# Performance work log

Hardware: AMD Instinct MI355X
Metric: run time of the kernel (lower is better)

Reference implementation:

```python
import jax, jax.numpy as jnp
import numpy as np

HID, H, D = 128, 4, 32
NB, NP, NC = 60000, 2000, 4000
EM, EP, EI = 150000, 300000, 150000


def segment_softmax(logits, seg, n):
    # logits: [E, H], seg: [E] destination ids
    m = jax.ops.segment_max(logits, seg, num_segments=n)
    m = jnp.where(jnp.isfinite(m), m, 0.0)  # guard empty segments
    e = jnp.exp(logits - m[seg])
    s = jax.ops.segment_sum(e, seg, num_segments=n)
    return e / (s[seg] + 1e-16)


def layer_norm(x, g, b):
    mu = x.mean(-1, keepdims=True)
    v = ((x - mu) ** 2).mean(-1, keepdims=True)
    return (x - mu) / jnp.sqrt(v + 1e-5) * g + b


def setup_inputs():
    key = jax.random.key(0)
    ks = jax.random.split(key, 40)
    i = iter(range(40))
    nrm = lambda shape, s=1.0: jax.random.normal(ks[next(i)], shape, jnp.float32) * s
    w = lambda shape: nrm(shape, 0.05)
    inp = {
        'x_ball': nrm((NB, HID)),
        'x_player': nrm((NP, HID)),
        'x_context': nrm((NC, HID)),
        'em': jnp.stack([jax.random.randint(ks[next(i)], (EM,), 0, NP),
                         jax.random.randint(ks[next(i)], (EM,), 0, NB)]),
        'ep': jnp.stack([jax.random.randint(ks[next(i)], (EP,), 0, NB),
                         jax.random.randint(ks[next(i)], (EP,), 0, NB)]),
        'ei': jnp.stack([jax.random.randint(ks[next(i)], (EI,), 0, NB),
                         jax.random.randint(ks[next(i)], (EI,), 0, NC)]),
        'ea_p': nrm((EP, 1)),
        # GATv2Conv (player -matchup-> ball)
        'g_Wl': w((HID, HID)), 'g_Wr': w((HID, HID)), 'g_att': w((H, D)), 'g_b': jnp.zeros((HID,), jnp.float32),
        # TransformerConv (ball -recent_precedes-> ball), edge_dim=1
        't_Wq': w((HID, HID)), 't_bq': jnp.zeros((HID,), jnp.float32),
        't_Wk': w((HID, HID)), 't_bk': jnp.zeros((HID,), jnp.float32),
        't_Wv': w((HID, HID)), 't_bv': jnp.zeros((HID,), jnp.float32),
        't_We': w((1, HID)),
        't_Wskip': w((HID, HID)), 't_bskip': jnp.zeros((HID,), jnp.float32),
        # SAGEConv mean (ball -informs-> context)
        's_Wl': w((HID, HID)), 's_bl': jnp.zeros((HID,), jnp.float32), 's_Wr': w((HID, HID)),
        # per-type LayerNorms (only applied to types produced by the conv)
        'ln_ball_g': jnp.ones((HID,), jnp.float32), 'ln_ball_b': jnp.zeros((HID,), jnp.float32),
        'ln_ctx_g': jnp.ones((HID,), jnp.float32), 'ln_ctx_b': jnp.zeros((HID,), jnp.float32),
    }
    return inp


def reference(x_ball, x_player, x_context, em, ep, ei, ea_p,
              g_Wl, g_Wr, g_att, g_b,
              t_Wq, t_bq, t_Wk, t_bk, t_Wv, t_bv, t_We, t_Wskip, t_bskip,
              s_Wl, s_bl, s_Wr,
              ln_ball_g, ln_ball_b, ln_ctx_g, ln_ctx_b):
    # ---- GATv2Conv: player -> ball ----
    src, dst = em[0], em[1]
    xl = (x_player @ g_Wl).reshape(NP, H, D)   # src transform
    xr = (x_ball @ g_Wr).reshape(NB, H, D)     # dst transform
    e = xl[src] + xr[dst]                      # [EM, H, D]
    e = jnp.where(e > 0, e, 0.2 * e)           # leaky_relu(0.2)
    logit = jnp.einsum('ehd,hd->eh', e, g_att)
    alpha = segment_softmax(logit, dst, NB)
    gat = jax.ops.segment_sum(xl[src] * alpha[..., None], dst, num_segments=NB)
    gat = gat.reshape(NB, HID) + g_b

    # ---- TransformerConv: ball -> ball, edge_dim=1 ----
    src, dst = ep[0], ep[1]
    q = (x_ball @ t_Wq + t_bq).reshape(NB, H, D)
    k = (x_ball @ t_Wk + t_bk).reshape(NB, H, D)
    v = (x_ball @ t_Wv + t_bv).reshape(NB, H, D)
    ee = (ea_p @ t_We).reshape(EP, H, D)       # lin_edge (no bias)
    kj = k[src] + ee
    logit = jnp.einsum('ehd,ehd->eh', q[dst], kj) / jnp.sqrt(jnp.float32(D))
    alpha = segment_softmax(logit, dst, NB)
    tr = jax.ops.segment_sum((v[src] + ee) * alpha[..., None], dst, num_segments=NB)
    tr = tr.reshape(NB, HID) + x_ball @ t_Wskip + t_bskip  # root/skip connection

    # ---- SAGEConv mean: ball -> context ----
    src, dst = ei[0], ei[1]
    summ = jax.ops.segment_sum(x_ball[src], dst, num_segments=NC)
    cnt = jax.ops.segment_sum(jnp.ones((EI,), jnp.float32), dst, num_segments=NC)
    mean = summ / jnp.maximum(cnt, 1.0)[:, None]
    sage = mean @ s_Wl + s_bl + x_context @ s_Wr

    # ---- HeteroConv aggr='sum' + residual + per-type LayerNorm ----
    ball_out = layer_norm(gat + tr + x_ball, ln_ball_g, ln_ball_b)
    ctx_out = layer_norm(sage + x_context, ln_ctx_g, ln_ctx_b)
    # 'player' receives no messages -> passed through unchanged
    return (ball_out, ctx_out, x_player)
```

## Files before the change

kernel.cpp:

```cpp
#include <hip/hip_runtime.h>
#include <hip/hip_bf16.h>

#define NB 60000
#define NP 2000
#define NC 4000
#define EM_N 150000
#define EP_N 300000
#define EI_N 150000
#define POOL_N (EM_N + EP_N + EI_N)
#define SEG_TOT (NB + NB + NC)
#define SCAN_BLK 1024
#define NPART ((SEG_TOT + SCAN_BLK - 1) / SCAN_BLK)
#define BALL_BLKS ((NB + 63) / 64)
#define PLYR_BLKS ((NP + 63) / 64)
#define CTXG_BLKS ((NC + 63) / 64)
#define GEMM_BLKS (BALL_BLKS + PLYR_BLKS + CTXG_BLKS)
#define FILL_BLKS ((POOL_N + 255) / 256)
#define COPY_BLKS ((NP * 128 + 255) / 256)
#define BBALL ((NB + 3) / 4)

typedef __hip_bfloat16 bf16;
typedef unsigned int u32;
typedef __attribute__((ext_vector_type(8))) short s8v;
typedef __attribute__((ext_vector_type(4))) float f4v;

__device__ __forceinline__ short f2bs(float f) {
    bf16 h = __float2bfloat16(f);
    return __builtin_bit_cast(short, h);
}
__device__ __forceinline__ float bsToF(short s) {
    return __builtin_bit_cast(float, ((unsigned)(unsigned short)s) << 16);
}
__device__ __forceinline__ float loF(u32 v) { return bsToF((short)(v & 0xffff)); }
__device__ __forceinline__ float hiF(u32 v) { return bsToF((short)(v >> 16)); }
__device__ __forceinline__ u32 packbf(float a, float b) {
    return (u32)(unsigned short)f2bs(a) | ((u32)(unsigned short)f2bs(b) << 16);
}
__device__ __forceinline__ void gl_lds16(const void* g, void* l) {
    __builtin_amdgcn_global_load_lds((const __attribute__((address_space(1))) void*)g,
                                     (__attribute__((address_space(3))) void*)l, 16, 0, 0);
}

__global__ void hist_wt_copy_kernel(const int* __restrict__ em, const int* __restrict__ ep,
                                    const int* __restrict__ ei, int* __restrict__ counts,
                                    const float* __restrict__ W0, const float* __restrict__ W1,
                                    const float* __restrict__ W2, const float* __restrict__ W3,
                                    const float* __restrict__ W4, const float* __restrict__ W5,
                                    const float* __restrict__ W6, const float* __restrict__ W7,
                                    ushort* __restrict__ Wt,
                                    const float* __restrict__ x_player, float* __restrict__ out) {
    if (blockIdx.x >= FILL_BLKS) {
        int t = (blockIdx.x - FILL_BLKS) * 256 + threadIdx.x;
        if (t < NP * 128) out[(size_t)(NB + NC) * 128 + t] = x_player[t];
        return;
    }
    int t = blockIdx.x * 256 + threadIdx.x;
    if (t < 8 * 16384) {
        int w = t >> 14, r = t & 16383, k = r >> 7, n = r & 127;
        const float* W = (w == 0) ? W0 : (w == 1) ? W1 : (w == 2) ? W2 : (w == 3) ? W3
                       : (w == 4) ? W4 : (w == 5) ? W5 : (w == 6) ? W6 : W7;
        int sc = (n >> 5) * 32 + ((n & 1) << 4) + ((n & 31) >> 1);
        Wt[w * 16384 + (k >> 3) * 1024 + sc * 8 + (k & 7)] = (unsigned short)f2bs(W[k * 128 + n]);
    }
    if (t < EM_N) atomicAdd(&counts[em[EM_N + t]], 1);
    else if (t < EM_N + EP_N) atomicAdd(&counts[NB + ep[EP_N + (t - EM_N)]], 1);
    else if (t < POOL_N) atomicAdd(&counts[2 * NB + ei[EI_N + (t - EM_N - EP_N)]], 1);
}

__global__ void scan_fused_kernel(const int* __restrict__ counts, int* __restrict__ offsets,
                                  int* __restrict__ cursors, int* __restrict__ gbase) {
    __shared__ int sd[256];
    __shared__ int sbase;
    int b = blockIdx.x, tid = threadIdx.x;
    int base = b * SCAN_BLK + tid * 4;
    int v[4]; int ts = 0;
#pragma unroll
    for (int j = 0; j < 4; j++) { int idx = base + j; v[j] = (idx < SEG_TOT) ? counts[idx] : 0; ts += v[j]; }
    sd[tid] = ts;
    for (int off = 1; off < 256; off <<= 1) {
        __syncthreads(); int t = (tid >= off) ? sd[tid - off] : 0;
        __syncthreads(); sd[tid] += t;
    }
    __syncthreads();
    if (tid == 255) sbase = atomicAdd(gbase, sd[255]);
    __syncthreads();
    int run = sd[tid] - ts + sbase;
#pragma unroll
    for (int j = 0; j < 4; j++) {
        int idx = base + j;
        if (idx < SEG_TOT) { offsets[idx] = run; cursors[idx] = run; }
        run += v[j];
    }
}

__device__ __forceinline__ void pass_compute(const ushort* __restrict__ lds, const s8v a[4],
                                             const float* __restrict__ bp,
                                             const float* __restrict__ Ares,
                                             int mbase, int M, int l16, int quad,
                                             u32* __restrict__ op) {
#pragma unroll
    for (int t = 0; t < 4; t++) {
        f4v alo = {0.f, 0.f, 0.f, 0.f}, ahi = {0.f, 0.f, 0.f, 0.f};
#pragma unroll
        for (int kt = 0; kt < 4; kt++) {
            s8v blo = *(const s8v*)(lds + (kt * 4 + quad) * 1024 + (t * 32 + l16) * 8);
            s8v bhi = *(const s8v*)(lds + (kt * 4 + quad) * 1024 + (t * 32 + 16 + l16) * 8);
            alo = __builtin_amdgcn_mfma_f32_16x16x32_bf16(a[kt], blo, alo, 0, 0, 0);
            ahi = __builtin_amdgcn_mfma_f32_16x16x32_bf16(a[kt], bhi, ahi, 0, 0, 0);
        }
        float bvlo = 0.f, bvhi = 0.f;
        if (bp) { float2 b2 = ((const float2*)bp)[t * 16 + l16]; bvlo = b2.x; bvhi = b2.y; }
#pragma unroll
        for (int r = 0; r < 4; r++) {
            int row = mbase + quad * 4 + r;
            if (row < M) {
                float vlo = alo[r] + bvlo, vhi = ahi[r] + bvhi;
                if (Ares) {
                    float2 xr2 = ((const float2*)Ares)[(size_t)row * 64 + t * 16 + l16];
                    vlo += xr2.x; vhi += xr2.y;
                }
                op[(size_t)row * 64 + t * 16 + l16] = packbf(vlo, vhi);
            }
        }
    }
}

__global__ __launch_bounds__(256) void gemm6_fill_kernel(
    const float* __restrict__ Aball, const float* __restrict__ Aplyr, const float* __restrict__ Actx,
    const ushort* __restrict__ Wt,
    const float* __restrict__ bq, const float* __restrict__ bk,
    const float* __restrict__ bv_, const float* __restrict__ bskip,
    const float* __restrict__ g_b, const float* __restrict__ bl,
    u32* __restrict__ xrP, u32* __restrict__ qP, uint2* __restrict__ kvP,
    u32* __restrict__ skipP, u32* __restrict__ xlP, u32* __restrict__ xwP,
    u32* __restrict__ ctxlinP,
    const int* __restrict__ em, const int* __restrict__ ep, const int* __restrict__ ei,
    const float* __restrict__ ea_p, int* __restrict__ cursors, int2* __restrict__ pool) {
    __shared__ ushort lds[16384];
    if (blockIdx.x >= GEMM_BLKS) {
        int t = (blockIdx.x - GEMM_BLKS) * 256 + threadIdx.x;
        int seg, s; float ea = 0.f;
        if (t < EM_N) { s = em[t]; seg = em[EM_N + t]; }
        else if (t < EM_N + EP_N) { int e = t - EM_N; s = ep[e]; seg = NB + ep[EP_N + e]; ea = ea_p[e]; }
        else if (t < POOL_N) { int e = t - EM_N - EP_N; s = ei[e]; seg = 2 * NB + ei[EI_N + e]; }
        else return;
        int pos = atomicAdd(&cursors[seg], 1);
        pool[pos] = make_int2(s, __float_as_int(ea));
        return;
    }
    const int tid = threadIdx.x;
    const int lane = tid & 63;
    const int wv = tid >> 6;
    const int quad = lane >> 4, l16 = lane & 15;
    int kind, bidx;
    if (blockIdx.x < BALL_BLKS) { kind = 0; bidx = blockIdx.x; }
    else if (blockIdx.x < BALL_BLKS + PLYR_BLKS) { kind = 1; bidx = blockIdx.x - BALL_BLKS; }
    else { kind = 2; bidx = blockIdx.x - BALL_BLKS - PLYR_BLKS; }
    const int M = (kind == 0) ? NB : (kind == 1) ? NP : NC;
    const float* A = (kind == 0) ? Aball : (kind == 1) ? Aplyr : Actx;
    const int mbase = bidx * 64 + wv * 16;
    const int ldsbase = wv * 512;

#define STAGE(W) do { \
    const ushort* _src = Wt + (W) * 16384; \
    _Pragma("unroll") \
    for (int p = 0; p < 8; p++) \
        gl_lds16(_src + (size_t)(p * 256 + tid) * 8, lds + p * 2048 + ldsbase); \
} while (0)

    STAGE(kind == 0 ? 0 : (kind == 1 ? 5 : 7));

    s8v a[4];
    {
        int row = mbase + l16;
        if (row >= M) row = M - 1;
        const float* ap = A + (size_t)row * 128 + quad * 8;
#pragma unroll
        for (int kt = 0; kt < 4; kt++) {
            const float4* p = (const float4*)(ap + kt * 32);
            float4 u = p[0], v = p[1];
            s8v f;
            f[0] = f2bs(u.x); f[1] = f2bs(u.y); f[2] = f2bs(u.z); f[3] = f2bs(u.w);
            f[4] = f2bs(v.x); f[5] = f2bs(v.y); f[6] = f2bs(v.z); f[7] = f2bs(v.w);
            a[kt] = f;
        }
    }
    __syncthreads();

    if (kind == 1) {
        pass_compute(lds, a, nullptr, nullptr, mbase, M, l16, quad, xlP);
        return;
    }
    if (kind == 2) {
        pass_compute(lds, a, bl, Actx, mbase, M, l16, quad, ctxlinP);
        return;
    }
    pass_compute(lds, a, nullptr, nullptr, mbase, M, l16, quad, xrP);
    __syncthreads(); STAGE(1); __syncthreads();
    pass_compute(lds, a, bq, nullptr, mbase, M, l16, quad, qP);
    __syncthreads(); STAGE(2); __syncthreads();
    u32 kpk[4][4];
#pragma unroll
    for (int t = 0; t < 4; t++) {
        f4v alo = {0.f, 0.f, 0.f, 0.f}, ahi = {0.f, 0.f, 0.f, 0.f};
#pragma unroll
        for (int kt = 0; kt < 4; kt++) {
            s8v blo = *(const s8v*)(lds + (kt * 4 + quad) * 1024 + (t * 32 + l16) * 8);
            s8v bhi = *(const s8v*)(lds + (kt * 4 + quad) * 1024 + (t * 32 + 16 + l16) * 8);
            alo = __builtin_amdgcn_mfma_f32_16x16x32_bf16(a[kt], blo, alo, 0, 0, 0);
            ahi = __builtin_amdgcn_mfma_f32_16x16x32_bf16(a[kt], bhi, ahi, 0, 0, 0);
        }
        float2 bk2 = ((const float2*)bk)[t * 16 + l16];
#pragma unroll
        for (int r = 0; r < 4; r++) kpk[t][r] = packbf(alo[r] + bk2.x, ahi[r] + bk2.y);
    }
    __syncthreads(); STAGE(3); __syncthreads();
#pragma unroll
    for (int t = 0; t < 4; t++) {
        f4v alo = {0.f, 0.f, 0.f, 0.f}, ahi = {0.f, 0.f, 0.f, 0.f};
#pragma unroll
        for (int kt = 0; kt < 4; kt++) {
            s8v blo = *(const s8v*)(lds + (kt * 4 + quad) * 1024 + (t * 32 + l16) * 8);
            s8v bhi = *(const s8v*)(lds + (kt * 4 + quad) * 1024 + (t * 32 + 16 + l16) * 8);
            alo = __builtin_amdgcn_mfma_f32_16x16x32_bf16(a[kt], blo, alo, 0, 0, 0);
            ahi = __builtin_amdgcn_mfma_f32_16x16x32_bf16(a[kt], bhi, ahi, 0, 0, 0);
        }
        float2 bv2 = ((const float2*)bv_)[t * 16 + l16];
#pragma unroll
        for (int r = 0; r < 4; r++) {
            int row = mbase + quad * 4 + r;
            if (row < NB)
                kvP[(size_t)row * 64 + t * 16 + l16] =
                    make_uint2(kpk[t][r], packbf(alo[r] + bv2.x, ahi[r] + bv2.y));
        }
    }
    __syncthreads(); STAGE(4); __syncthreads();
    pass_compute(lds, a, bskip, Aball, mbase, M, l16, quad, skipP);
    __syncthreads(); STAGE(6); __syncthreads();
    pass_compute(lds, a, nullptr, nullptr, mbase, M, l16, quad, xwP);
#undef STAGE
}

__global__ __launch_bounds__(256) void ball_sage_kernel(
    const u32* __restrict__ xlP, const u32* __restrict__ xrP, const u32* __restrict__ qP,
    const uint2* __restrict__ kvP, const u32* __restrict__ skipP, const u32* __restrict__ xwP,
    const u32* __restrict__ ctxlinP,
    const float* __restrict__ g_att, const float* __restrict__ g_b, const float* __restrict__ We,
    const int* __restrict__ offsets, const int* __restrict__ counts,
    const int2* __restrict__ pool,
    const float* __restrict__ ln_g, const float* __restrict__ ln_b,
    const float* __restrict__ cg, const float* __restrict__ cb,
    float* __restrict__ out) {
    __shared__ float part[4][128];
    const int wv = threadIdx.x >> 6, l = threadIdx.x & 63;

    if (blockIdx.x >= BBALL) {
        int c = blockIdx.x - BBALL;
        int beg = offsets[2 * NB + c], cnt = counts[2 * NB + c];
        float s0 = 0.f, s1 = 0.f;
        for (int j = wv; j < cnt; j += 4) {
            u32 xv = xwP[(size_t)pool[beg + j].x * 64 + l];
            s0 += loF(xv); s1 += hiF(xv);
        }
        part[wv][l * 2] = s0; part[wv][l * 2 + 1] = s1;
        __syncthreads();
        if (wv == 0) {
            float m = fmaxf((float)cnt, 1.f);
            u32 cl = ctxlinP[(size_t)c * 64 + l];
            float v0 = (part[0][l * 2] + part[1][l * 2] + part[2][l * 2] + part[3][l * 2]) / m + loF(cl);
            float v1 = (part[0][l * 2 + 1] + part[1][l * 2 + 1] + part[2][l * 2 + 1] + part[3][l * 2 + 1]) / m + hiF(cl);
            float s = v0 + v1;
#pragma unroll
            for (int m2 = 1; m2 <= 32; m2 <<= 1) s += __shfl_xor(s, m2);
            float mu = s * (1.f / 128.f);
            float d0 = v0 - mu, d1 = v1 - mu;
            float qv = d0 * d0 + d1 * d1;
#pragma unroll
            for (int m2 = 1; m2 <= 32; m2 <<= 1) qv += __shfl_xor(qv, m2);
            float inv = rsqrtf(qv * (1.f / 128.f) + 1e-5f);
            float2 g2 = ((const float2*)cg)[l];
            float2 b2 = ((const float2*)cb)[l];
            ((float2*)out)[(size_t)(NB + c) * 64 + l] =
                make_float2(d0 * inv * g2.x + b2.x, d1 * inv * g2.y + b2.y);
        }
        return;
    }

    const int d = blockIdx.x * 4 + wv;
    const size_t rowD = (size_t)d * 64;

    float2 att = ((const float2*)g_att)[l];
    u32 xr2 = xrP[rowD + l];
    float xr0 = loF(xr2), xr1 = hiF(xr2);
    int beg = offsets[d], cnt = counts[d];
    float n0 = 0.f, n1 = 0.f, deg = 0.f;
    for (int j = 0; j < cnt; j += 4) {
        int sI[4]; bool ok[4];
#pragma unroll
        for (int i = 0; i < 4; i++) {
            ok[i] = (j + i < cnt);
            sI[i] = ok[i] ? pool[beg + j + i].x : 0;
        }
        u32 xv[4];
#pragma unroll
        for (int i = 0; i < 4; i++) xv[i] = xlP[(size_t)sI[i] * 64 + l];
        float p[4], xa[4], xb[4];
#pragma unroll
        for (int i = 0; i < 4; i++) {
            xa[i] = loF(xv[i]); xb[i] = hiF(xv[i]);
            float u0 = xa[i] + xr0; u0 = u0 > 0.f ? u0 : 0.2f * u0;
            float u1 = xb[i] + xr1; u1 = u1 > 0.f ? u1 : 0.2f * u1;
            p[i] = u0 * att.x + u1 * att.y;
        }
#pragma unroll
        for (int m = 1; m <= 8; m <<= 1) {
#pragma unroll
            for (int i = 0; i < 4; i++) p[i] += __shfl_xor(p[i], m);
        }
#pragma unroll
        for (int i = 0; i < 4; i++) {
            p[i] = ok[i] ? __expf(p[i]) : 0.f;
            n0 += p[i] * xa[i]; n1 += p[i] * xb[i]; deg += p[i];
        }
    }
    float gat0 = n0 / (deg + 1e-16f), gat1 = n1 / (deg + 1e-16f);

    u32 q2 = qP[rowD + l];
    float q0 = loF(q2), q1 = hiF(q2);
    float2 we = ((const float2*)We)[l];
    float dw = q0 * we.x + q1 * we.y;
#pragma unroll
    for (int m = 1; m <= 8; m <<= 1) dw += __shfl_xor(dw, m);
    beg = offsets[NB + d]; cnt = counts[NB + d];
    float sv0 = 0.f, sv1 = 0.f, spe = 0.f, det = 0.f;
    for (int j = 0; j < cnt; j += 4) {
        int2 pr[4]; bool ok[4];
#pragma unroll
        for (int i = 0; i < 4; i++) {
            ok[i] = (j + i < cnt);
            pr[i] = ok[i] ? pool[beg + j + i] : make_int2(0, 0);
        }
        uint2 kv[4];
#pragma unroll
        for (int i = 0; i < 4; i++) kv[i] = kvP[(size_t)pr[i].x * 64 + l];
        float p[4], ea[4];
#pragma unroll
        for (int i = 0; i < 4; i++) {
            ea[i] = __int_as_float(pr[i].y);
            p[i] = q0 * loF(kv[i].x) + q1 * hiF(kv[i].x);
        }
#pragma unroll
        for (int m = 1; m <= 8; m <<= 1) {
#pragma unroll
            for (int i = 0; i < 4; i++) p[i] += __shfl_xor(p[i], m);
        }
#pragma unroll
        for (int i = 0; i < 4; i++) {
            p[i] = ok[i] ? __expf((p[i] + ea[i] * dw) * 0.17677669529663687f) : 0.f;
            sv0 += p[i] * loF(kv[i].y); sv1 += p[i] * hiF(kv[i].y);
            spe += p[i] * ea[i]; det += p[i];
        }
    }
    float tr0 = (sv0 + spe * we.x) / (det + 1e-16f);
    float tr1 = (sv1 + spe * we.y) / (det + 1e-16f);

    u32 sk = skipP[rowD + l];
    float2 gb2 = ((const float2*)g_b)[l];
    float val0 = loF(sk) + gb2.x + gat0 + tr0;
    float val1 = hiF(sk) + gb2.y + gat1 + tr1;
    float s = val0 + val1;
#pragma unroll
    for (int m = 1; m <= 32; m <<= 1) s += __shfl_xor(s, m);
    float mu = s * (1.f / 128.f);
    float d0 = val0 - mu, d1 = val1 - mu;
    float qv = d0 * d0 + d1 * d1;
#pragma unroll
    for (int m = 1; m <= 32; m <<= 1) qv += __shfl_xor(qv, m);
    float inv = rsqrtf(qv * (1.f / 128.f) + 1e-5f);
    float2 g2 = ((const float2*)ln_g)[l];
    float2 b2 = ((const float2*)ln_b)[l];
    ((float2*)out)[rowD + l] = make_float2(d0 * inv * g2.x + b2.x, d1 * inv * g2.y + b2.y);
}

extern "C" void kernel_launch(void* const* d_in, const int* in_sizes, int n_in,
                              void* d_out, int out_size, void* d_ws, size_t ws_size,
                              hipStream_t stream) {
    const float* x_ball = (const float*)d_in[0];
    const float* x_player = (const float*)d_in[1];
    const float* x_context = (const float*)d_in[2];
    const int* em = (const int*)d_in[3];
    const int* ep = (const int*)d_in[4];
    const int* ei = (const int*)d_in[5];
    const float* ea_p = (const float*)d_in[6];
    const float* g_Wl = (const float*)d_in[7];
    const float* g_Wr = (const float*)d_in[8];
    const float* g_att = (const float*)d_in[9];
    const float* g_b = (const float*)d_in[10];
    const float* t_Wq = (const float*)d_in[11];
    const float* t_bq = (const float*)d_in[12];
    const float* t_Wk = (const float*)d_in[13];
    const float* t_bk = (const float*)d_in[14];
    const float* t_Wv = (const float*)d_in[15];
    const float* t_bv = (const float*)d_in[16];
    const float* t_We = (const float*)d_in[17];
    const float* t_Wskip = (const float*)d_in[18];
    const float* t_bskip = (const float*)d_in[19];
    const float* s_Wl = (const float*)d_in[20];
    const float* s_bl = (const float*)d_in[21];
    const float* s_Wr = (const float*)d_in[22];
    const float* ln_ball_g = (const float*)d_in[23];
    const float* ln_ball_b = (const float*)d_in[24];
    const float* ln_ctx_g = (const float*)d_in[25];
    const float* ln_ctx_b = (const float*)d_in[26];
    float* out = (float*)d_out;

    float* ws = (float*)d_ws;
    size_t o = 0;
    int* counts = (int*)(ws + o);   o += SEG_TOT;
    int* gbase = (int*)(ws + o);    o += 1;
    int* offsets = (int*)(ws + o);  o += SEG_TOT;
    int* cursors = (int*)(ws + o);  o += SEG_TOT;
    if (o & 1) o++;
    int2* pool = (int2*)(ws + o);   o += (size_t)POOL_N * 2;
    o = (o + 3) & ~(size_t)3;
    ushort* Wt = (ushort*)(ws + o); o += (8 * 16384) / 2;
    u32* xlP = (u32*)(ws + o);      o += (size_t)NP * 64;
    u32* xrP = (u32*)(ws + o);      o += (size_t)NB * 64;
    u32* qP = (u32*)(ws + o);       o += (size_t)NB * 64;
    u32* skipP = (u32*)(ws + o);    o += (size_t)NB * 64;
    u32* xwP = (u32*)(ws + o);      o += (size_t)NB * 64;
    u32* ctxlinP = (u32*)(ws + o);  o += (size_t)NC * 64;
    if (o & 1) o++;
    uint2* kvP = (uint2*)(ws + o);  o += (size_t)NB * 128;

    dim3 blk(256);
    hipMemsetAsync(counts, 0, (SEG_TOT + 1) * sizeof(int), stream);
    hist_wt_copy_kernel<<<FILL_BLKS + COPY_BLKS, blk, 0, stream>>>(
        em, ep, ei, counts, g_Wr, t_Wq, t_Wk, t_Wv, t_Wskip, g_Wl, s_Wl, s_Wr, Wt, x_player, out);
    scan_fused_kernel<<<NPART, blk, 0, stream>>>(counts, offsets, cursors, gbase);
    gemm6_fill_kernel<<<GEMM_BLKS + FILL_BLKS, blk, 0, stream>>>(
        x_ball, x_player, x_context, Wt, t_bq, t_bk, t_bv, t_bskip, g_b, s_bl,
        xrP, qP, kvP, skipP, xlP, xwP, ctxlinP, em, ep, ei, ea_p, cursors, pool);
    ball_sage_kernel<<<BBALL + NC, blk, 0, stream>>>(
        xlP, xrP, qP, kvP, skipP, xwP, ctxlinP, g_att, g_b, t_We,
        offsets, counts, pool, ln_ball_g, ln_ball_b, ln_ctx_g, ln_ctx_b, out);
}
```

Baseline: 305.3 us.

## Double-buffer weight staging and prefetch gather indices/rows in ball aggregation

The GEMM kernel now double-buffers the weight tiles in LDS, issuing the next weight load before computing the current pass, which removes one barrier per pass. Q is prescaled by 1/sqrt(D)*log2e and the attention vector by log2e so the softmax can use exp2f. The ball aggregation kernel now loads the first 8 pool entries and their feature rows for both GAT and Transformer up front, overlapping the two gathers. The SAGE mean loop is software-pipelined two entries ahead. This raises register and LDS pressure, and bf16 rounding of the prescaled q changes numerics slightly.

New measurement: 301.3 us. No clear change (-1.3%).

```diff
diff --git a/kernel.cpp b/kernel.cpp
--- a/kernel.cpp
+++ b/kernel.cpp
@@ -19,6 +19,9 @@
 #define COPY_BLKS ((NP * 128 + 255) / 256)
 #define BBALL ((NB + 3) / 4)
 
+#define QSCALE (0.17677669529663687f * 1.4426950408889634f)
+#define LOG2E 1.4426950408889634f
+
 typedef __hip_bfloat16 bf16;
 typedef unsigned int u32;
 typedef __attribute__((ext_vector_type(8))) short s8v;
@@ -93,9 +96,9 @@
     }
 }
 
-__device__ __forceinline__ void pass_compute(const ushort* __restrict__ lds, const s8v a[4],
+__device__ __forceinline__ void pass_compute(const ushort* __restrict__ ldsb, const s8v a[4],
                                              const float* __restrict__ bp,
-                                             const float* __restrict__ Ares,
+                                             const float* __restrict__ Ares, float scale,
                                              int mbase, int M, int l16, int quad,
                                              u32* __restrict__ op) {
 #pragma unroll
@@ -103,8 +106,8 @@
         f4v alo = {0.f, 0.f, 0.f, 0.f}, ahi = {0.f, 0.f, 0.f, 0.f};
 #pragma unroll
         for (int kt = 0; kt < 4; kt++) {
-            s8v blo = *(const s8v*)(lds + (kt * 4 + quad) * 1024 + (t * 32 + l16) * 8);
-            s8v bhi = *(const s8v*)(lds + (kt * 4 + quad) * 1024 + (t * 32 + 16 + l16) * 8);
+            s8v blo = *(const s8v*)(ldsb + (kt * 4 + quad) * 1024 + (t * 32 + l16) * 8);
+            s8v bhi = *(const s8v*)(ldsb + (kt * 4 + quad) * 1024 + (t * 32 + 16 + l16) * 8);
             alo = __builtin_amdgcn_mfma_f32_16x16x32_bf16(a[kt], blo, alo, 0, 0, 0);
             ahi = __builtin_amdgcn_mfma_f32_16x16x32_bf16(a[kt], bhi, ahi, 0, 0, 0);
         }
@@ -114,7 +117,7 @@
         for (int r = 0; r < 4; r++) {
             int row = mbase + quad * 4 + r;
             if (row < M) {
-                float vlo = alo[r] + bvlo, vhi = ahi[r] + bvhi;
+                float vlo = (alo[r] + bvlo) * scale, vhi = (ahi[r] + bvhi) * scale;
                 if (Ares) {
                     float2 xr2 = ((const float2*)Ares)[(size_t)row * 64 + t * 16 + l16];
                     vlo += xr2.x; vhi += xr2.y;
@@ -136,7 +139,7 @@
     u32* __restrict__ ctxlinP,
     const int* __restrict__ em, const int* __restrict__ ep, const int* __restrict__ ei,
     const float* __restrict__ ea_p, int* __restrict__ cursors, int2* __restrict__ pool) {
-    __shared__ ushort lds[16384];
+    __shared__ ushort lds[2][16384];
     if (blockIdx.x >= GEMM_BLKS) {
         int t = (blockIdx.x - GEMM_BLKS) * 256 + threadIdx.x;
         int seg, s; float ea = 0.f;
@@ -161,14 +164,14 @@
     const int mbase = bidx * 64 + wv * 16;
     const int ldsbase = wv * 512;
 
-#define STAGE(W) do { \
+#define STAGE(W, BUF) do { \
     const ushort* _src = Wt + (W) * 16384; \
     _Pragma("unroll") \
     for (int p = 0; p < 8; p++) \
-        gl_lds16(_src + (size_t)(p * 256 + tid) * 8, lds + p * 2048 + ldsbase); \
+        gl_lds16(_src + (size_t)(p * 256 + tid) * 8, (BUF) + p * 2048 + ldsbase); \
 } while (0)
 
-    STAGE(kind == 0 ? 0 : (kind == 1 ? 5 : 7));
+    STAGE(kind == 0 ? 0 : (kind == 1 ? 5 : 7), lds[0]);
 
     s8v a[4];
     {
@@ -188,25 +191,28 @@
     __syncthreads();
 
     if (kind == 1) {
-        pass_compute(lds, a, nullptr, nullptr, mbase, M, l16, quad, xlP);
+        pass_compute(lds[0], a, nullptr, nullptr, 1.f, mbase, M, l16, quad, xlP);
         return;
     }
     if (kind == 2) {
-        pass_compute(lds, a, bl, Actx, mbase, M, l16, quad, ctxlinP);
+        pass_compute(lds[0], a, bl, Actx, 1.f, mbase, M, l16, quad, ctxlinP);
         return;
     }
-    pass_compute(lds, a, nullptr, nullptr, mbase, M, l16, quad, xrP);
-    __syncthreads(); STAGE(1); __syncthreads();
-    pass_compute(lds, a, bq, nullptr, mbase, M, l16, quad, qP);
-    __syncthreads(); STAGE(2); __syncthreads();
+    STAGE(1, lds[1]);
+    pass_compute(lds[0], a, nullptr, nullptr, 1.f, mbase, M, l16, quad, xrP);
+    __syncthreads();
+    STAGE(2, lds[0]);
+    pass_compute(lds[1], a, bq, nullptr, QSCALE, mbase, M, l16, quad, qP);
+    __syncthreads();
+    STAGE(3, lds[1]);
     u32 kpk[4][4];
 #pragma unroll
     for (int t = 0; t < 4; t++) {
         f4v alo = {0.f, 0.f, 0.f, 0.f}, ahi = {0.f, 0.f, 0.f, 0.f};
 #pragma unroll
         for (int kt = 0; kt < 4; kt++) {
-            s8v blo = *(const s8v*)(lds + (kt * 4 + quad) * 1024 + (t * 32 + l16) * 8);
-            s8v bhi = *(const s8v*)(lds + (kt * 4 + quad) * 1024 + (t * 32 + 16 + l16) * 8);
+            s8v blo = *(const s8v*)(lds[0] + (kt * 4 + quad) * 1024 + (t * 32 + l16) * 8);
+            s8v bhi = *(const s8v*)(lds[0] + (kt * 4 + quad) * 1024 + (t * 32 + 16 + l16) * 8);
             alo = __builtin_amdgcn_mfma_f32_16x16x32_bf16(a[kt], blo, alo, 0, 0, 0);
             ahi = __builtin_amdgcn_mfma_f32_16x16x32_bf16(a[kt], bhi, ahi, 0, 0, 0);
         }
@@ -214,14 +220,15 @@
 #pragma unroll
         for (int r = 0; r < 4; r++) kpk[t][r] = packbf(alo[r] + bk2.x, ahi[r] + bk2.y);
     }
-    __syncthreads(); STAGE(3); __syncthreads();
+    __syncthreads();
+    STAGE(4, lds[0]);
 #pragma unroll
     for (int t = 0; t < 4; t++) {
         f4v alo = {0.f, 0.f, 0.f, 0.f}, ahi = {0.f, 0.f, 0.f, 0.f};
 #pragma unroll
         for (int kt = 0; kt < 4; kt++) {
-            s8v blo = *(const s8v*)(lds + (kt * 4 + quad) * 1024 + (t * 32 + l16) * 8);
-            s8v bhi = *(const s8v*)(lds + (kt * 4 + quad) * 1024 + (t * 32 + 16 + l16) * 8);
+            s8v blo = *(const s8v*)(lds[1] + (kt * 4 + quad) * 1024 + (t * 32 + l16) * 8);
+            s8v bhi = *(const s8v*)(lds[1] + (kt * 4 + quad) * 1024 + (t * 32 + 16 + l16) * 8);
             alo = __builtin_amdgcn_mfma_f32_16x16x32_bf16(a[kt], blo, alo, 0, 0, 0);
             ahi = __builtin_amdgcn_mfma_f32_16x16x32_bf16(a[kt], bhi, ahi, 0, 0, 0);
         }
@@ -234,11 +241,54 @@
                     make_uint2(kpk[t][r], packbf(alo[r] + bv2.x, ahi[r] + bv2.y));
         }
     }
-    __syncthreads(); STAGE(4); __syncthreads();
-    pass_compute(lds, a, bskip, Aball, mbase, M, l16, quad, skipP);
-    __syncthreads(); STAGE(6); __syncthreads();
-    pass_compute(lds, a, nullptr, nullptr, mbase, M, l16, quad, xwP);
+    __syncthreads();
+    STAGE(6, lds[1]);
+    pass_compute(lds[0], a, bskip, Aball, 1.f, mbase, M, l16, quad, skipP);
+    __syncthreads();
+    pass_compute(lds[1], a, nullptr, nullptr, 1.f, mbase, M, l16, quad, xwP);
 #undef STAGE
+}
+
+__device__ __forceinline__ void gat_batch(const u32 xv[4], const bool ok[4],
+                                          float xr0, float xr1, float attx, float atty,
+                                          float& n0, float& n1, float& deg) {
+    float p[4], xa[4], xb[4];
+#pragma unroll
+    for (int i = 0; i < 4; i++) {
+        xa[i] = loF(xv[i]); xb[i] = hiF(xv[i]);
+        float u0 = xa[i] + xr0; u0 = u0 > 0.f ? u0 : 0.2f * u0;
+        float u1 = xb[i] + xr1; u1 = u1 > 0.f ? u1 : 0.2f * u1;
+        p[i] = u0 * attx + u1 * atty;
+    }
+#pragma unroll
+    for (int m = 1; m <= 8; m <<= 1) {
+#pragma unroll
+        for (int i = 0; i < 4; i++) p[i] += __shfl_xor(p[i], m);
+    }
+#pragma unroll
+    for (int i = 0; i < 4; i++) {
+        p[i] = ok[i] ? exp2f(p[i]) : 0.f;
+        n0 += p[i] * xa[i]; n1 += p[i] * xb[i]; deg += p[i];
+    }
+}
+
+__device__ __forceinline__ void tr_batch(const uint2 kv[4], const float ea[4], const bool ok[4],
+                                         float q0, float q1, float dw,
+                                         float& sv0, float& sv1, float& spe, float& det) {
+    float p[4];
+#pragma unroll
+    for (int i = 0; i < 4; i++) p[i] = q0 * loF(kv[i].x) + q1 * hiF(kv[i].x);
+#pragma unroll
+    for (int m = 1; m <= 8; m <<= 1) {
+#pragma unroll
+        for (int i = 0; i < 4; i++) p[i] += __shfl_xor(p[i], m);
+    }
+#pragma unroll
+    for (int i = 0; i < 4; i++) {
+        p[i] = ok[i] ? exp2f(p[i] + ea[i] * dw) : 0.f;
+        sv0 += p[i] * loF(kv[i].y); sv1 += p[i] * hiF(kv[i].y);
+        spe += p[i] * ea[i]; det += p[i];
+    }
 }
 
 __global__ __launch_bounds__(256) void ball_sage_kernel(
@@ -258,9 +308,20 @@
         int c = blockIdx.x - BBALL;
         int beg = offsets[2 * NB + c], cnt = counts[2 * NB + c];
         float s0 = 0.f, s1 = 0.f;
-        for (int j = wv; j < cnt; j += 4) {
-            u32 xv = xwP[(size_t)pool[beg + j].x * 64 + l];
-            s0 += loF(xv); s1 += hiF(xv);
+        int j = wv;
+        if (j < cnt) {
+            int i0 = pool[beg + j].x;
+            int idx1 = (j + 4 < cnt) ? beg + j + 4 : 0;
+            int i1 = pool[idx1].x;
+            u32 x0 = xwP[(size_t)i0 * 64 + l];
+            u32 x1 = xwP[(size_t)i1 * 64 + l];
+            for (; j < cnt; j += 4) {
+                int idx2 = (j + 8 < cnt) ? beg + j + 8 : 0;
+                int i2 = pool[idx2].x;
+                s0 += loF(x0); s1 += hiF(x0);
+                x0 = x1;
+                x1 = xwP[(size_t)i2 * 64 + l];
+            }
         }
         part[wv][l * 2] = s0; part[wv][l * 2 + 1] = s1;
         __syncthreads();
@@ -288,83 +349,105 @@
 
     const int d = blockIdx.x * 4 + wv;
     const size_t rowD = (size_t)d * 64;
-
-    float2 att = ((const float2*)g_att)[l];
+    const int ds = __builtin_amdgcn_readfirstlane(d);
+
     u32 xr2 = xrP[rowD + l];
-    float xr0 = loF(xr2), xr1 = hiF(xr2);
-    int beg = offsets[d], cnt = counts[d];
-    float n0 = 0.f, n1 = 0.f, deg = 0.f;
-    for (int j = 0; j < cnt; j += 4) {
-        int sI[4]; bool ok[4];
-#pragma unroll
-        for (int i = 0; i < 4; i++) {
-            ok[i] = (j + i < cnt);
-            sI[i] = ok[i] ? pool[beg + j + i].x : 0;
-        }
-        u32 xv[4];
-#pragma unroll
-        for (int i = 0; i < 4; i++) xv[i] = xlP[(size_t)sI[i] * 64 + l];
-        float p[4], xa[4], xb[4];
-#pragma unroll
-        for (int i = 0; i < 4; i++) {
-            xa[i] = loF(xv[i]); xb[i] = hiF(xv[i]);
-            float u0 = xa[i] + xr0; u0 = u0 > 0.f ? u0 : 0.2f * u0;
-            float u1 = xb[i] + xr1; u1 = u1 > 0.f ? u1 : 0.2f * u1;
-            p[i] = u0 * att.x + u1 * att.y;
-        }
-#pragma unroll
-        for (int m = 1; m <= 8; m <<= 1) {
-#pragma unroll
-            for (int i = 0; i < 4; i++) p[i] += __shfl_xor(p[i], m);
-        }
-#pragma unroll
-        for (int i = 0; i < 4; i++) {
-            p[i] = ok[i] ? __expf(p[i]) : 0.f;
-            n0 += p[i] * xa[i]; n1 += p[i] * xb[i]; deg += p[i];
-        }
-    }
-    float gat0 = n0 / (deg + 1e-16f), gat1 = n1 / (deg + 1e-16f);
-
     u32 q2 = qP[rowD + l];
+    u32 sk = skipP[rowD + l];
+
+    const int begG = offsets[ds], cntG = counts[ds];
+    const int begT = offsets[NB + ds], cntT = counts[NB + ds];
+    int gS[8];
+#pragma unroll
+    for (int i = 0; i < 8; i++) { int idx = (i < cntG) ? begG + i : 0; gS[i] = pool[idx].x; }
+    int tS[8]; float tE[8];
+#pragma unroll
+    for (int i = 0; i < 8; i++) {
+        int idx = (i < cntT) ? begT + i : 0;
+        int2 pr = pool[idx]; tS[i] = pr.x; tE[i] = __int_as_float(pr.y);
+    }
+
+    u32 gx[8];
+    if (cntG > 0) {
+#pragma unroll
+        for (int i = 0; i < 4; i++) gx[i] = xlP[(size_t)gS[i] * 64 + l];
+        if (cntG > 4) {
+#pragma unroll
+            for (int i = 4; i < 8; i++) gx[i] = xlP[(size_t)gS[i] * 64 + l];
+        }
+    }
+    uint2 kva[8];
+    if (cntT > 0) {
+#pragma unroll
+        for (int i = 0; i < 4; i++) kva[i] = kvP[(size_t)tS[i] * 64 + l];
+        if (cntT > 4) {
+#pragma unroll
+            for (int i = 4; i < 8; i++) kva[i] = kvP[(size_t)tS[i] * 64 + l];
+        }
+    }
+
     float q0 = loF(q2), q1 = hiF(q2);
     float2 we = ((const float2*)We)[l];
     float dw = q0 * we.x + q1 * we.y;
 #pragma unroll
     for (int m = 1; m <= 8; m <<= 1) dw += __shfl_xor(dw, m);
-    beg = offsets[NB + d]; cnt = counts[NB + d];
+
+    float2 attv = ((const float2*)g_att)[l];
+    float attx = attv.x * LOG2E, atty = attv.y * LOG2E;
+    float xr0 = loF(xr2), xr1 = hiF(xr2);
+    float n0 = 0.f, n1 = 0.f, deg = 0.f;
+    if (cntG > 0) {
+        bool ok[4];
+#pragma unroll
+        for (int i = 0; i < 4; i++) ok[i] = (i < cntG);
+        gat_batch(&gx[0], ok, xr0, xr1, attx, atty, n0, n1, deg);
+        if (cntG > 4) {
+            bool ok2[4];
+#pragma unroll
+            for (int i = 0; i < 4; i++) ok2[i] = (4 + i < cntG);
+            gat_batch(&gx[4], ok2, xr0, xr1, attx, atty, n0, n1, deg);
+        }
+        for (int j = 8; j < cntG; j += 4) {
+            bool ok3[4]; u32 xv[4];
+#pragma unroll
+            for (int i = 0; i < 4; i++) {
+                ok3[i] = (j + i < cntG);
+                int idx = ok3[i] ? begG + j + i : 0;
+                xv[i] = xlP[(size_t)pool[idx].x * 64 + l];
+            }
+            gat_batch(xv, ok3, xr0, xr1, attx, atty, n0, n1, deg);
+        }
+    }
+    float gat0 = n0 / (deg + 1e-16f), gat1 = n1 / (deg + 1e-16f);
+
     float sv0 = 0.f, sv1 = 0.f, spe = 0.f, det = 0.f;
-    for (int j = 0; j < cnt; j += 4) {
-        int2 pr[4]; bool ok[4];
-#pragma unroll
-        for (int i = 0; i < 4; i++) {
-            ok[i] = (j + i < cnt);
-            pr[i] = ok[i] ? pool[beg + j + i] : make_int2(0, 0);
-        }
-        uint2 kv[4];
-#pragma unroll
-        for (int i = 0; i < 4; i++) kv[i] = kvP[(size_t)pr[i].x * 64 + l];
-        float p[4], ea[4];
-#pragma unroll
-        for (int i = 0; i < 4; i++) {
-            ea[i] = __int_as_float(pr[i].y);
-            p[i] = q0 * loF(kv[i].x) + q1 * hiF(kv[i].x);
-        }
-#pragma unroll
-        for (int m = 1; m <= 8; m <<= 1) {
-#pragma unroll
-            for (int i = 0; i < 4; i++) p[i] += __shfl_xor(p[i], m);
-        }
-#pragma unroll
-        for (int i = 0; i < 4; i++) {
-            p[i] = ok[i] ? __expf((p[i] + ea[i] * dw) * 0.17677669529663687f) : 0.f;
-            sv0 += p[i] * loF(kv[i].y); sv1 += p[i] * hiF(kv[i].y);
-            spe += p[i] * ea[i]; det += p[i];
+    if (cntT > 0) {
+        bool ok[4];
+#pragma unroll
+        for (int i = 0; i < 4; i++) ok[i] = (i < cntT);
+        tr_batch(&kva[0], &tE[0], ok, q0, q1, dw, sv0, sv1, spe, det);
+        if (cntT > 4) {
+            bool ok2[4];
+#pragma unroll
+            for (int i = 0; i < 4; i++) ok2[i] = (4 + i < cntT);
+            tr_batch(&kva[4], &tE[4], ok2, q0, q1, dw, sv0, sv1, spe, det);
+        }
+        for (int j = 8; j < cntT; j += 4) {
+            bool ok3[4]; uint2 kv[4]; float ea[4];
+#pragma unroll
+            for (int i = 0; i < 4; i++) {
+                ok3[i] = (j + i < cntT);
+                int idx = ok3[i] ? begT + j + i : 0;
+                int2 pr = pool[idx];
+                ea[i] = __int_as_float(pr.y);
+                kv[i] = kvP[(size_t)pr.x * 64 + l];
+            }
+            tr_batch(kv, ea, ok3, q0, q1, dw, sv0, sv1, spe, det);
         }
     }
     float tr0 = (sv0 + spe * we.x) / (det + 1e-16f);
     float tr1 = (sv1 + spe * we.y) / (det + 1e-16f);
 
-    u32 sk = skipP[rowD + l];
     float2 gb2 = ((const float2*)g_b)[l];
     float val0 = loF(sk) + gb2.x + gat0 + tr0;
     float val1 = hiF(sk) + gb2.y + gat1 + tr1;
```
